# Kernel optimization log

Measured on AMD Instinct MI355X. Metric: run time of the kernel, lower is better.

The kernel has to match this reference:

```python
import jax, jax.numpy as jnp
from jax import lax
import numpy as np

B, S, H, L = 64, 512, 768, 9

def setup_inputs() -> dict:
    key = jax.random.key(0)
    ks = jax.random.split(key, 8)
    return {
        'hidden': jax.random.normal(ks[0], (B, S, H), dtype=jnp.float32),
        'W': jax.random.normal(ks[1], (H, L), dtype=jnp.float32) * 0.02,
        'b': jax.random.normal(ks[2], (L,), dtype=jnp.float32) * 0.02,
        'start_transitions': jax.random.normal(ks[3], (L,), dtype=jnp.float32) * 0.1,
        'transitions': jax.random.normal(ks[4], (L, L), dtype=jnp.float32) * 0.1,
        'end_transitions': jax.random.normal(ks[5], (L,), dtype=jnp.float32) * 0.1,
        'labels': jax.random.randint(ks[6], (B, S), 0, L, dtype=jnp.int64),
        'lengths': jax.random.randint(ks[7], (B,), 0, S, dtype=jnp.int32),
    }

def _crf_nll(emissions, labels, mask, start_transitions, transitions, end_transitions):
    # emissions [B,S,L], labels [B,S] int, mask [B,S] bool (mask[:,0] all True)
    Bv = emissions.shape[0]
    bidx = jnp.arange(Bv)
    fmask = mask.astype(emissions.dtype)
    # --- numerator: score of the gold path ---
    t0 = labels[:, 0]
    score0 = start_transitions[t0] + emissions[bidx, 0, t0]  # [B]
    def num_step(score, xs):
        em_t, tag_prev, tag_t, m_t = xs  # [B,L],[B],[B],[B]
        inc = transitions[tag_prev, tag_t] + em_t[bidx, tag_t]
        return score + inc * m_t, None
    num_xs = (jnp.swapaxes(emissions[:, 1:], 0, 1),  # [S-1,B,L]
              labels[:, :-1].T, labels[:, 1:].T, fmask[:, 1:].T)
    numerator, _ = lax.scan(num_step, score0, num_xs)
    seq_ends = jnp.sum(mask, axis=1) - 1  # [B]
    last_tags = labels[bidx, seq_ends]
    numerator = numerator + end_transitions[last_tags]
    # --- denominator: forward algorithm (logsumexp DP) ---
    alpha0 = start_transitions[None, :] + emissions[:, 0]  # [B,L]
    def den_step(alpha, xs):
        em_t, m_t = xs  # [B,L], [B] bool
        nxt = jax.scipy.special.logsumexp(
            alpha[:, :, None] + transitions[None, :, :] + em_t[:, None, :], axis=1)
        return jnp.where(m_t[:, None], nxt, alpha), None
    den_xs = (jnp.swapaxes(emissions[:, 1:], 0, 1), mask[:, 1:].T)
    alpha, _ = lax.scan(den_step, alpha0, den_xs)
    denominator = jax.scipy.special.logsumexp(alpha + end_transitions[None, :], axis=1)
    # torchcrf forward returns sum of log-likelihoods (reduction='sum'); model negates
    return -jnp.sum(numerator - denominator)

def reference(hidden, W, b, start_transitions, transitions, end_transitions, labels, lengths):
    # dropout is identity at inference; BERT output is modeled by `hidden`
    emissions = jnp.einsum('bsh,hl->bsl', hidden, W) + b  # [B,S,L]
    lens = jnp.maximum(lengths, 1)  # torchcrf requires mask[:,0] on
    mask = jnp.arange(emissions.shape[1])[None, :] < lens[:, None]  # [B,S]
    return _crf_nll(emissions, labels, mask, start_transitions, transitions, end_transitions)
```

## Files before the change

kernel.cpp:

```cpp
#include <hip/hip_runtime.h>

#define B_ 64
#define S_ 512
#define H_ 768
#define L_ 9
#define EMP 16
#define CH 16
#define NCHUNK 32
#define CPAD 88

typedef __attribute__((ext_vector_type(8))) short bf16x8;
typedef __attribute__((ext_vector_type(4))) float f32x4;

__device__ __forceinline__ int eoff(int t) { return t * 12 + (t >> 4) * 4; }

__device__ __forceinline__ unsigned pack_bf16(float lo, float hi) {
    unsigned a = __float_as_uint(lo) + 0x8000u;
    unsigned b = __float_as_uint(hi) + 0x8000u;
    return __builtin_amdgcn_perm(b, a, 0x07060302);
}

__global__ __launch_bounds__(256) void emis_kernel(
    const float* __restrict__ hidden, const float* __restrict__ W,
    const float* __restrict__ bias, const int* __restrict__ lengths,
    float* __restrict__ em, float* __restrict__ out)
{
    __shared__ unsigned Wl[96 * 16 * 4];
    __shared__ float bias16[16];

    const int T = threadIdx.x;
    if (blockIdx.x == 0 && T == 0) out[0] = 0.0f;

    const int row0 = blockIdx.x * 64;
    const int b = row0 >> 9;
    int len = lengths[b]; if (len < 1) len = 1;
    if ((row0 & 511) >= len) return;

    const int wv = T >> 6, lane = T & 63;
    const int r0 = row0 + wv * 16;
    const int q = lane >> 4, col = lane & 15;
    const bool tile_live = ((r0 & 511) < len);

    const float* hp = hidden + (size_t)(r0 + col) * H_ + q * 8;
    float4 ph[8];
    if (tile_live) {
        #pragma unroll
        for (int st = 0; st < 4; ++st) {
            ph[2 * st]     = *(const float4*)(hp + st * 32);
            ph[2 * st + 1] = *(const float4*)(hp + st * 32 + 4);
        }
    }

    if (T < 16) bias16[T] = (T < 9) ? bias[T] : 0.0f;
    #pragma unroll
    for (int r6 = 0; r6 < 6; ++r6) {
        const int sidx = T + 256 * r6;
        const int k8 = sidx >> 4, c = sidx & 15;
        unsigned w0 = 0, w1 = 0, w2 = 0, w3 = 0;
        if (c < 9) {
            const float* wp = W + (size_t)(k8 * 8) * 9 + c;
            w0 = pack_bf16(wp[0],  wp[9]);
            w1 = pack_bf16(wp[18], wp[27]);
            w2 = pack_bf16(wp[36], wp[45]);
            w3 = pack_bf16(wp[54], wp[63]);
        }
        uint4 v = { w0, w1, w2, w3 };
        *(uint4*)&Wl[sidx * 4] = v;
    }
    __syncthreads();

    if (!tile_live) return;

    const float4 bias4 = *(const float4*)(bias16 + q * 4);

    f32x4 acc = { 0.0f, 0.0f, 0.0f, 0.0f };
    #pragma unroll
    for (int st = 0; st < 24; ++st) {
        float4 h0, h1;
        if (st < 4) { h0 = ph[2 * st]; h1 = ph[2 * st + 1]; }
        else {
            h0 = *(const float4*)(hp + st * 32);
            h1 = *(const float4*)(hp + st * 32 + 4);
        }
        union { unsigned u[4]; bf16x8 v; } bu, au;
        bu.u[0] = pack_bf16(h0.x, h0.y);
        bu.u[1] = pack_bf16(h0.z, h0.w);
        bu.u[2] = pack_bf16(h1.x, h1.y);
        bu.u[3] = pack_bf16(h1.z, h1.w);
        const uint4 a4 = *(const uint4*)&Wl[((st * 4 + q) * 16 + col) * 4];
        au.u[0] = a4.x; au.u[1] = a4.y; au.u[2] = a4.z; au.u[3] = a4.w;
        acc = __builtin_amdgcn_mfma_f32_16x16x32_bf16(au.v, bu.v, acc, 0, 0, 0);
    }

    const int srow = (r0 & 511) + col;
    if (srow < len) {
        float4 o = { acc[0] + bias4.x, acc[1] + bias4.y,
                     acc[2] + bias4.z, acc[3] + bias4.w };
        *(float4*)(em + (size_t)((b << 9) + srow) * EMP + q * 4) = o;
    }
}

__global__ __launch_bounds__(384, 1) void crf_kernel(
    const float* __restrict__ em, const int* __restrict__ labels,
    const int* __restrict__ lengths, const float* __restrict__ start_t,
    const float* __restrict__ trans, const float* __restrict__ end_t,
    float* __restrict__ out)
{
    __shared__ float eem[6288];
    __shared__ float Pl[112];
    __shared__ float Cs[NCHUNK * CPAD];
    __shared__ float Cs2[16 * CPAD];
    __shared__ float rmx_s[16 * 12];
    __shared__ float lgA[32], lgB[16];
    const int T = threadIdx.x;
    const int b = blockIdx.x;
    int len = lengths[b]; if (len < 1) len = 1;

    if (T < 81) {
        const int k = T / 9, j = T - 9 * k;
        Pl[k * 12 + j] = __expf(trans[T]);
    }
    #pragma unroll
    for (int r = 0; r < 2; ++r) {
        const int t = T + 384 * r;
        if (t < len) {
            const int o = eoff(t);
            const float4* p = (const float4*)(em + (size_t)((b << 9) + t) * EMP);
            float4 v0 = p[0], v1 = p[1], v2 = p[2];
            float4 w0 = { __expf(v0.x), __expf(v0.y), __expf(v0.z), __expf(v0.w) };
            float4 w1 = { __expf(v1.x), __expf(v1.y), __expf(v1.z), __expf(v1.w) };
            *(float4*)(eem + o) = w0;
            *(float4*)(eem + o + 4) = w1;
            eem[o + 8] = __expf(v2.x);
        }
    }
    if (T < 32) lgA[T] = 0.0f;
    __syncthreads();

    if (T < 288) {
        const int c = T / 9;
        const int i = T - 9 * c;
        float A[9];
        #pragma unroll
        for (int j = 0; j < 9; ++j) A[j] = (i == j) ? 1.0f : 0.0f;
        const int t0 = CH * c + 1;

        #pragma unroll 1
        for (int s = 0; s < CH; ++s) {
            const int t = t0 + s;
            const int o = eoff(t);
            float4 e0 = *(const float4*)(eem + o);
            float4 e1 = *(const float4*)(eem + o + 4);
            const float e8 = eem[o + 8];
            const float e[9] = { e0.x, e0.y, e0.z, e0.w,
                                 e1.x, e1.y, e1.z, e1.w, e8 };

            float an[9];
            #pragma unroll
            for (int j = 0; j < 9; ++j) an[j] = 0.0f;
            #pragma unroll
            for (int k = 0; k < 9; ++k) {
                float4 p0 = *(const float4*)(Pl + k * 12);
                float4 p1 = *(const float4*)(Pl + k * 12 + 4);
                const float p8 = Pl[k * 12 + 8];
                const float pr[9] = { p0.x, p0.y, p0.z, p0.w,
                                      p1.x, p1.y, p1.z, p1.w, p8 };
                const float ak = A[k];
                #pragma unroll
                for (int j = 0; j < 9; ++j)
                    an[j] = fmaf(ak, pr[j], an[j]);
            }
            const bool live = (t < len);
            #pragma unroll
            for (int j = 0; j < 9; ++j)
                A[j] = live ? an[j] * e[j] : A[j];
            if (s == 7) {
                #pragma unroll
                for (int j = 0; j < 9; ++j) A[j] *= 0x1p-40f;
            }
        }
        #pragma unroll
        for (int j = 0; j < 9; ++j) Cs[c * CPAD + i * 9 + j] = A[j];
    } else if (T >= 320) {
        const int lane = T - 320;
        const int* lab = labels + (size_t)b * S_;
        float part = 0.0f;
        for (int t = 1 + lane; t < len; t += 64) {
            const int tp = lab[t - 1], tc = lab[t];
            part += trans[tp * 9 + tc] + em[(size_t)((b << 9) + t) * EMP + tc];
        }
        #pragma unroll
        for (int off = 32; off >= 1; off >>= 1) part += __shfl_xor(part, off, 64);
        if (lane == 0) {
            const int l0 = lab[0], le = lab[len - 1];
            const float num = start_t[l0] + em[(size_t)(b << 9) * EMP + l0]
                            + part + end_t[le];
            atomicAdd(out, -num);
        }
    }
    __syncthreads();

    float* src = Cs;  float* dst = Cs2;
    float* ls  = lgA; float* ld  = lgB;
    int nn = 16;
    #pragma unroll 1
    for (int lvl = 0; lvl < 5; ++lvl) {
        const int n = T / 9, i = T - 9 * n;
        float row[9];
        if (T < nn * 9) {
            const float* Am = src + (2 * n) * CPAD;
            const float* Bm = src + (2 * n + 1) * CPAD;
            float a[9];
            #pragma unroll
            for (int k = 0; k < 9; ++k) a[k] = Am[i * 9 + k];
            #pragma unroll
            for (int j = 0; j < 9; ++j) row[j] = 0.0f;
            #pragma unroll
            for (int k = 0; k < 9; ++k) {
                const float ak = a[k];
                #pragma unroll
                for (int j = 0; j < 9; ++j)
                    row[j] = fmaf(ak, Bm[k * 9 + j], row[j]);
            }
            float rmx = row[0];
            #pragma unroll
            for (int j = 1; j < 9; ++j) rmx = fmaxf(rmx, row[j]);
            rmx_s[n * 12 + i] = rmx;
        }
        __syncthreads();
        if (T < nn * 9) {
            float mx = rmx_s[n * 12];
            #pragma unroll
            for (int k = 1; k < 9; ++k) mx = fmaxf(mx, rmx_s[n * 12 + k]);
            const float inv = 1.0f / mx;
            #pragma unroll
            for (int j = 0; j < 9; ++j) dst[n * CPAD + i * 9 + j] = row[j] * inv;
            if (i == 0) ld[n] = ls[2 * n] + ls[2 * n + 1] + __logf(mx);
        }
        __syncthreads();
        float* t1 = src; src = dst; dst = t1;
        float* t2 = ls;  ls = ld;  ld = t2;
        nn >>= 1;
    }

    if (T == 0) {
        const float4* e0 = (const float4*)(em + (size_t)(b << 9) * EMP);
        float4 v0 = e0[0], v1 = e0[1], v2 = e0[2];
        float al[9] = { v0.x + start_t[0], v0.y + start_t[1], v0.z + start_t[2],
                        v0.w + start_t[3], v1.x + start_t[4], v1.y + start_t[5],
                        v1.z + start_t[6], v1.w + start_t[7], v2.x + start_t[8] };
        float m0 = al[0];
        #pragma unroll
        for (int j = 1; j < 9; ++j) m0 = fmaxf(m0, al[j]);
        float alpha[9];
        #pragma unroll
        for (int j = 0; j < 9; ++j) alpha[j] = __expf(al[j] - m0);

        float ev = 0.0f;
        #pragma unroll
        for (int j = 0; j < 9; ++j) {
            float s = 0.0f;
            #pragma unroll
            for (int i = 0; i < 9; ++i)
                s = fmaf(alpha[i], src[i * 9 + j], s);
            ev = fmaf(s, __expf(end_t[j]), ev);
        }
        const float den = m0 + ls[0] + __logf(ev)
                        + 1280.0f * 0.6931471805599453f;
        atomicAdd(out, den);
    }
}

extern "C" void kernel_launch(void* const* d_in, const int* in_sizes, int n_in,
                              void* d_out, int out_size, void* d_ws, size_t ws_size,
                              hipStream_t stream)
{
    (void)in_sizes; (void)n_in; (void)out_size; (void)ws_size;
    const float* hidden  = (const float*)d_in[0];
    const float* W       = (const float*)d_in[1];
    const float* bias    = (const float*)d_in[2];
    const float* start_t = (const float*)d_in[3];
    const float* trans   = (const float*)d_in[4];
    const float* end_t   = (const float*)d_in[5];
    const int*   labels  = (const int*)d_in[6];
    const int*   lengths = (const int*)d_in[7];

    float* em  = (float*)d_ws;
    float* out = (float*)d_out;

    emis_kernel<<<512, 256, 0, stream>>>(hidden, W, bias, lengths, em, out);
    crf_kernel<<<B_, 384, 0, stream>>>(em, labels, lengths,
                                       start_t, trans, end_t, out);
}
```

Measured before the change: 32.88 us.

## Split emission GEMM along hidden dim into two partial buffers summed in CRF

The emission kernel now splits the 768-wide reduction into two halves handled by separate blocks, doubling the grid to 1024 blocks. Each half writes a partial emission buffer, and the CRF kernel sums the two partials when it loads emissions. The aim is more parallelism and more memory requests in flight for the bandwidth-bound hidden read. The cost is extra workspace, twice the emission write and read traffic, and an extra add per element in the CRF kernel.

Measured after the change: 32.01 us, median of 2. 2.7% less time.

```diff
diff --git a/kernel.cpp b/kernel.cpp
--- a/kernel.cpp
+++ b/kernel.cpp
@@ -23,15 +23,17 @@
 __global__ __launch_bounds__(256) void emis_kernel(
     const float* __restrict__ hidden, const float* __restrict__ W,
     const float* __restrict__ bias, const int* __restrict__ lengths,
-    float* __restrict__ em, float* __restrict__ out)
+    float* __restrict__ em0, float* __restrict__ em1, float* __restrict__ out)
 {
-    __shared__ unsigned Wl[96 * 16 * 4];
+    __shared__ unsigned Wl[48 * 16 * 4];
     __shared__ float bias16[16];
 
     const int T = threadIdx.x;
     if (blockIdx.x == 0 && T == 0) out[0] = 0.0f;
 
-    const int row0 = blockIdx.x * 64;
+    const int kh  = blockIdx.x & 1;
+    const int grp = blockIdx.x >> 1;
+    const int row0 = grp * 64;
     const int b = row0 >> 9;
     int len = lengths[b]; if (len < 1) len = 1;
     if ((row0 & 511) >= len) return;
@@ -41,7 +43,7 @@
     const int q = lane >> 4, col = lane & 15;
     const bool tile_live = ((r0 & 511) < len);
 
-    const float* hp = hidden + (size_t)(r0 + col) * H_ + q * 8;
+    const float* hp = hidden + (size_t)(r0 + col) * H_ + kh * 384 + q * 8;
     float4 ph[8];
     if (tile_live) {
         #pragma unroll
@@ -51,14 +53,14 @@
         }
     }
 
-    if (T < 16) bias16[T] = (T < 9) ? bias[T] : 0.0f;
+    if (T < 16) bias16[T] = (kh == 0 && T < 9) ? bias[T] : 0.0f;
     #pragma unroll
-    for (int r6 = 0; r6 < 6; ++r6) {
-        const int sidx = T + 256 * r6;
-        const int k8 = sidx >> 4, c = sidx & 15;
+    for (int r3 = 0; r3 < 3; ++r3) {
+        const int sidx = T + 256 * r3;
+        const int k8l = sidx >> 4, c = sidx & 15;
         unsigned w0 = 0, w1 = 0, w2 = 0, w3 = 0;
         if (c < 9) {
-            const float* wp = W + (size_t)(k8 * 8) * 9 + c;
+            const float* wp = W + (size_t)(kh * 384 + k8l * 8) * 9 + c;
             w0 = pack_bf16(wp[0],  wp[9]);
             w1 = pack_bf16(wp[18], wp[27]);
             w2 = pack_bf16(wp[36], wp[45]);
@@ -75,7 +77,7 @@
 
     f32x4 acc = { 0.0f, 0.0f, 0.0f, 0.0f };
     #pragma unroll
-    for (int st = 0; st < 24; ++st) {
+    for (int st = 0; st < 12; ++st) {
         float4 h0, h1;
         if (st < 4) { h0 = ph[2 * st]; h1 = ph[2 * st + 1]; }
         else {
@@ -94,17 +96,18 @@
 
     const int srow = (r0 & 511) + col;
     if (srow < len) {
+        float* dst = (kh ? em1 : em0) + (size_t)((b << 9) + srow) * EMP + q * 4;
         float4 o = { acc[0] + bias4.x, acc[1] + bias4.y,
                      acc[2] + bias4.z, acc[3] + bias4.w };
-        *(float4*)(em + (size_t)((b << 9) + srow) * EMP + q * 4) = o;
+        *(float4*)dst = o;
     }
 }
 
 __global__ __launch_bounds__(384, 1) void crf_kernel(
-    const float* __restrict__ em, const int* __restrict__ labels,
-    const int* __restrict__ lengths, const float* __restrict__ start_t,
-    const float* __restrict__ trans, const float* __restrict__ end_t,
-    float* __restrict__ out)
+    const float* __restrict__ em0, const float* __restrict__ em1,
+    const int* __restrict__ labels, const int* __restrict__ lengths,
+    const float* __restrict__ start_t, const float* __restrict__ trans,
+    const float* __restrict__ end_t, float* __restrict__ out)
 {
     __shared__ float eem[6288];
     __shared__ float Pl[112];
@@ -125,13 +128,18 @@
         const int t = T + 384 * r;
         if (t < len) {
             const int o = eoff(t);
-            const float4* p = (const float4*)(em + (size_t)((b << 9) + t) * EMP);
-            float4 v0 = p[0], v1 = p[1], v2 = p[2];
-            float4 w0 = { __expf(v0.x), __expf(v0.y), __expf(v0.z), __expf(v0.w) };
-            float4 w1 = { __expf(v1.x), __expf(v1.y), __expf(v1.z), __expf(v1.w) };
+            const size_t off = (size_t)((b << 9) + t) * EMP;
+            const float4* p0 = (const float4*)(em0 + off);
+            const float4* p1 = (const float4*)(em1 + off);
+            float4 a0 = p0[0], a1 = p0[1], a2 = p0[2];
+            float4 b0 = p1[0], b1 = p1[1], b2 = p1[2];
+            float4 w0 = { __expf(a0.x + b0.x), __expf(a0.y + b0.y),
+                          __expf(a0.z + b0.z), __expf(a0.w + b0.w) };
+            float4 w1 = { __expf(a1.x + b1.x), __expf(a1.y + b1.y),
+                          __expf(a1.z + b1.z), __expf(a1.w + b1.w) };
             *(float4*)(eem + o) = w0;
             *(float4*)(eem + o + 4) = w1;
-            eem[o + 8] = __expf(v2.x);
+            eem[o + 8] = __expf(a2.x + b2.x);
         }
     }
     if (T < 32) lgA[T] = 0.0f;
@@ -187,13 +195,15 @@
         float part = 0.0f;
         for (int t = 1 + lane; t < len; t += 64) {
             const int tp = lab[t - 1], tc = lab[t];
-            part += trans[tp * 9 + tc] + em[(size_t)((b << 9) + t) * EMP + tc];
+            const size_t idx = (size_t)((b << 9) + t) * EMP + tc;
+            part += trans[tp * 9 + tc] + em0[idx] + em1[idx];
         }
         #pragma unroll
         for (int off = 32; off >= 1; off >>= 1) part += __shfl_xor(part, off, 64);
         if (lane == 0) {
             const int l0 = lab[0], le = lab[len - 1];
-            const float num = start_t[l0] + em[(size_t)(b << 9) * EMP + l0]
+            const size_t i0 = (size_t)(b << 9) * EMP + l0;
+            const float num = start_t[l0] + em0[i0] + em1[i0]
                             + part + end_t[le];
             atomicAdd(out, -num);
         }
@@ -244,11 +254,16 @@
     }
 
     if (T == 0) {
-        const float4* e0 = (const float4*)(em + (size_t)(b << 9) * EMP);
-        float4 v0 = e0[0], v1 = e0[1], v2 = e0[2];
-        float al[9] = { v0.x + start_t[0], v0.y + start_t[1], v0.z + start_t[2],
-                        v0.w + start_t[3], v1.x + start_t[4], v1.y + start_t[5],
-                        v1.z + start_t[6], v1.w + start_t[7], v2.x + start_t[8] };
+        const size_t off0 = (size_t)(b << 9) * EMP;
+        const float4* p0 = (const float4*)(em0 + off0);
+        const float4* p1 = (const float4*)(em1 + off0);
+        float4 a0 = p0[0], a1 = p0[1], a2 = p0[2];
+        float4 b0 = p1[0], b1 = p1[1], b2 = p1[2];
+        float al[9] = { a0.x + b0.x + start_t[0], a0.y + b0.y + start_t[1],
+                        a0.z + b0.z + start_t[2], a0.w + b0.w + start_t[3],
+                        a1.x + b1.x + start_t[4], a1.y + b1.y + start_t[5],
+                        a1.z + b1.z + start_t[6], a1.w + b1.w + start_t[7],
+                        a2.x + b2.x + start_t[8] };
         float m0 = al[0];
         #pragma unroll
         for (int j = 1; j < 9; ++j) m0 = fmaxf(m0, al[j]);
@@ -285,10 +300,12 @@
     const int*   labels  = (const int*)d_in[6];
     const int*   lengths = (const int*)d_in[7];
 
-    float* em  = (float*)d_ws;
+    float* em0 = (float*)d_ws;
+    float* em1 = em0 + (size_t)B_ * S_ * EMP;
     float* out = (float*)d_out;
 
-    emis_kernel<<<512, 256, 0, stream>>>(hidden, W, bias, lengths, em, out);
-    crf_kernel<<<B_, 384, 0, stream>>>(em, labels, lengths,
+    emis_kernel<<<1024, 256, 0, stream>>>(hidden, W, bias, lengths,
+                                          em0, em1, out);
+    crf_kernel<<<B_, 384, 0, stream>>>(em0, em1, labels, lengths,
                                        start_t, trans, end_t, out);
 }
```

## Fuse CRF chunk transfer-matrix products and gold-path scoring into emission kernel

Applied to the files above, without the earlier changes.

The per-chunk 9x9 transfer-matrix products and the numerator (gold-path) partial sums now run inside the emission GEMM blocks, straight from emissions held in shared memory. Each block writes 4 chunk matrices and a numerator partial to workspace. The CRF kernel then only loads the chunk matrices, substituting scaled identity matrices for dead chunks, and runs the log-depth tree reduction. This removes the round trip of the full emission tensor through global memory and the serial per-chunk loop in the 64-block CRF kernel, at the cost of longer emission blocks and an extra small workspace read.

New measurement: 32.60 us (median of 2 runs). About the same (-0.8%).

```diff
diff --git a/kernel.cpp b/kernel.cpp
--- a/kernel.cpp
+++ b/kernel.cpp
@@ -4,15 +4,10 @@
 #define S_ 512
 #define H_ 768
 #define L_ 9
-#define EMP 16
-#define CH 16
-#define NCHUNK 32
 #define CPAD 88
 
 typedef __attribute__((ext_vector_type(8))) short bf16x8;
 typedef __attribute__((ext_vector_type(4))) float f32x4;
-
-__device__ __forceinline__ int eoff(int t) { return t * 12 + (t >> 4) * 4; }
 
 __device__ __forceinline__ unsigned pack_bf16(float lo, float hi) {
     unsigned a = __float_as_uint(lo) + 0x8000u;
@@ -23,22 +18,31 @@
 __global__ __launch_bounds__(256) void emis_kernel(
     const float* __restrict__ hidden, const float* __restrict__ W,
     const float* __restrict__ bias, const int* __restrict__ lengths,
-    float* __restrict__ em, float* __restrict__ out)
+    const int* __restrict__ labels, const float* __restrict__ start_t,
+    const float* __restrict__ trans, const float* __restrict__ end_t,
+    float* __restrict__ Crec, float* __restrict__ em_row0,
+    float* __restrict__ num_part, float* __restrict__ out)
 {
     __shared__ unsigned Wl[96 * 16 * 4];
+    __shared__ float em_t[64 * 12];
+    __shared__ float ee_t[64 * 12];
+    __shared__ float Pl[112];
     __shared__ float bias16[16];
 
     const int T = threadIdx.x;
-    if (blockIdx.x == 0 && T == 0) out[0] = 0.0f;
-
-    const int row0 = blockIdx.x * 64;
-    const int b = row0 >> 9;
+    const int g = blockIdx.x;
+    const int b = g >> 3;
+    const int s0 = (g & 7) * 64;
+    if (g == 0 && T == 0) out[0] = 0.0f;
     int len = lengths[b]; if (len < 1) len = 1;
-    if ((row0 & 511) >= len) return;
+    if (s0 >= len) {
+        if (T == 0) num_part[g] = 0.0f;
+        return;
+    }
 
     const int wv = T >> 6, lane = T & 63;
-    const int r0 = row0 + wv * 16;
     const int q = lane >> 4, col = lane & 15;
+    const int r0 = g * 64 + wv * 16;
     const bool tile_live = ((r0 & 511) < len);
 
     const float* hp = hidden + (size_t)(r0 + col) * H_ + q * 8;
@@ -52,6 +56,7 @@
     }
 
     if (T < 16) bias16[T] = (T < 9) ? bias[T] : 0.0f;
+    if (T < 81) Pl[(T / 9) * 12 + (T % 9)] = __expf(trans[T]);
     #pragma unroll
     for (int r6 = 0; r6 < 6; ++r6) {
         const int sidx = T + 256 * r6;
@@ -69,92 +74,60 @@
     }
     __syncthreads();
 
-    if (!tile_live) return;
-
-    const float4 bias4 = *(const float4*)(bias16 + q * 4);
-
-    f32x4 acc = { 0.0f, 0.0f, 0.0f, 0.0f };
-    #pragma unroll
-    for (int st = 0; st < 24; ++st) {
-        float4 h0, h1;
-        if (st < 4) { h0 = ph[2 * st]; h1 = ph[2 * st + 1]; }
-        else {
-            h0 = *(const float4*)(hp + st * 32);
-            h1 = *(const float4*)(hp + st * 32 + 4);
-        }
-        union { unsigned u[4]; bf16x8 v; } bu, au;
-        bu.u[0] = pack_bf16(h0.x, h0.y);
-        bu.u[1] = pack_bf16(h0.z, h0.w);
-        bu.u[2] = pack_bf16(h1.x, h1.y);
-        bu.u[3] = pack_bf16(h1.z, h1.w);
-        const uint4 a4 = *(const uint4*)&Wl[((st * 4 + q) * 16 + col) * 4];
-        au.u[0] = a4.x; au.u[1] = a4.y; au.u[2] = a4.z; au.u[3] = a4.w;
-        acc = __builtin_amdgcn_mfma_f32_16x16x32_bf16(au.v, bu.v, acc, 0, 0, 0);
-    }
-
-    const int srow = (r0 & 511) + col;
-    if (srow < len) {
-        float4 o = { acc[0] + bias4.x, acc[1] + bias4.y,
-                     acc[2] + bias4.z, acc[3] + bias4.w };
-        *(float4*)(em + (size_t)((b << 9) + srow) * EMP + q * 4) = o;
-    }
-}
-
-__global__ __launch_bounds__(384, 1) void crf_kernel(
-    const float* __restrict__ em, const int* __restrict__ labels,
-    const int* __restrict__ lengths, const float* __restrict__ start_t,
-    const float* __restrict__ trans, const float* __restrict__ end_t,
-    float* __restrict__ out)
-{
-    __shared__ float eem[6288];
-    __shared__ float Pl[112];
-    __shared__ float Cs[NCHUNK * CPAD];
-    __shared__ float Cs2[16 * CPAD];
-    __shared__ float rmx_s[16 * 12];
-    __shared__ float lgA[32], lgB[16];
-    const int T = threadIdx.x;
-    const int b = blockIdx.x;
-    int len = lengths[b]; if (len < 1) len = 1;
-
-    if (T < 81) {
-        const int k = T / 9, j = T - 9 * k;
-        Pl[k * 12 + j] = __expf(trans[T]);
-    }
-    #pragma unroll
-    for (int r = 0; r < 2; ++r) {
-        const int t = T + 384 * r;
-        if (t < len) {
-            const int o = eoff(t);
-            const float4* p = (const float4*)(em + (size_t)((b << 9) + t) * EMP);
-            float4 v0 = p[0], v1 = p[1], v2 = p[2];
-            float4 w0 = { __expf(v0.x), __expf(v0.y), __expf(v0.z), __expf(v0.w) };
-            float4 w1 = { __expf(v1.x), __expf(v1.y), __expf(v1.z), __expf(v1.w) };
-            *(float4*)(eem + o) = w0;
-            *(float4*)(eem + o + 4) = w1;
-            eem[o + 8] = __expf(v2.x);
-        }
-    }
-    if (T < 32) lgA[T] = 0.0f;
+    if (tile_live) {
+        f32x4 acc = { 0.0f, 0.0f, 0.0f, 0.0f };
+        #pragma unroll
+        for (int st = 0; st < 24; ++st) {
+            float4 h0, h1;
+            if (st < 4) { h0 = ph[2 * st]; h1 = ph[2 * st + 1]; }
+            else {
+                h0 = *(const float4*)(hp + st * 32);
+                h1 = *(const float4*)(hp + st * 32 + 4);
+            }
+            union { unsigned u[4]; bf16x8 v; } bu, au;
+            bu.u[0] = pack_bf16(h0.x, h0.y);
+            bu.u[1] = pack_bf16(h0.z, h0.w);
+            bu.u[2] = pack_bf16(h1.x, h1.y);
+            bu.u[3] = pack_bf16(h1.z, h1.w);
+            const uint4 a4 = *(const uint4*)&Wl[((st * 4 + q) * 16 + col) * 4];
+            au.u[0] = a4.x; au.u[1] = a4.y; au.u[2] = a4.z; au.u[3] = a4.w;
+            acc = __builtin_amdgcn_mfma_f32_16x16x32_bf16(au.v, bu.v, acc, 0, 0, 0);
+        }
+        if (q < 3) {
+            const float4 b4 = *(const float4*)(bias16 + q * 4);
+            float4 o = { acc[0] + b4.x, acc[1] + b4.y,
+                         acc[2] + b4.z, acc[3] + b4.w };
+            *(float4*)&em_t[(wv * 16 + col) * 12 + q * 4] = o;
+        }
+    }
     __syncthreads();
 
-    if (T < 288) {
-        const int c = T / 9;
-        const int i = T - 9 * c;
+    if (T < 192) {
+        #pragma unroll
+        for (int k = 0; k < 3; ++k) {
+            const int idx = T + 192 * k;
+            const int r = idx / 9, c = idx - 9 * r;
+            ee_t[r * 12 + c] = __expf(em_t[r * 12 + c]);
+        }
+    }
+    __syncthreads();
+
+    if (T < 36) {
+        const int cl = T / 9, i = T - 9 * cl;
+        const int cg = 4 * (g & 7) + cl;
         float A[9];
         #pragma unroll
         for (int j = 0; j < 9; ++j) A[j] = (i == j) ? 1.0f : 0.0f;
-        const int t0 = CH * c + 1;
 
         #pragma unroll 1
-        for (int s = 0; s < CH; ++s) {
-            const int t = t0 + s;
-            const int o = eoff(t);
-            float4 e0 = *(const float4*)(eem + o);
-            float4 e1 = *(const float4*)(eem + o + 4);
-            const float e8 = eem[o + 8];
+        for (int s = 0; s < 16; ++s) {
+            const int t = 16 * cg + s;
+            const int r = 16 * cl + s;
+            float4 e0 = *(const float4*)&ee_t[r * 12];
+            float4 e1 = *(const float4*)&ee_t[r * 12 + 4];
+            const float e8 = ee_t[r * 12 + 8];
             const float e[9] = { e0.x, e0.y, e0.z, e0.w,
                                  e1.x, e1.y, e1.z, e1.w, e8 };
-
             float an[9];
             #pragma unroll
             for (int j = 0; j < 9; ++j) an[j] = 0.0f;
@@ -170,7 +143,7 @@
                 for (int j = 0; j < 9; ++j)
                     an[j] = fmaf(ak, pr[j], an[j]);
             }
-            const bool live = (t < len);
+            const bool live = (t >= 1) && (t < len);
             #pragma unroll
             for (int j = 0; j < 9; ++j)
                 A[j] = live ? an[j] * e[j] : A[j];
@@ -179,25 +152,60 @@
                 for (int j = 0; j < 9; ++j) A[j] *= 0x1p-40f;
             }
         }
-        #pragma unroll
-        for (int j = 0; j < 9; ++j) Cs[c * CPAD + i * 9 + j] = A[j];
-    } else if (T >= 320) {
-        const int lane = T - 320;
-        const int* lab = labels + (size_t)b * S_;
+        float* rec = Crec + ((size_t)b * 32 + cg) * CPAD + i * 9;
+        #pragma unroll
+        for (int j = 0; j < 9; ++j) rec[j] = A[j];
+    } else if (T >= 36 && T < 45) {
+        if (s0 == 0) em_row0[b * 12 + (T - 36)] = em_t[T - 36];
+    } else if (T >= 64 && T < 128) {
+        const int ln = T - 64;
+        const int t = s0 + ln;
         float part = 0.0f;
-        for (int t = 1 + lane; t < len; t += 64) {
-            const int tp = lab[t - 1], tc = lab[t];
-            part += trans[tp * 9 + tc] + em[(size_t)((b << 9) + t) * EMP + tc];
+        if (t >= 1 && t < len) {
+            const int tp = labels[b * S_ + t - 1];
+            const int tc = labels[b * S_ + t];
+            part = trans[tp * 9 + tc] + em_t[ln * 12 + tc];
+        }
+        if (ln == 0) {
+            if (s0 == 0) {
+                const int l0 = labels[b * S_];
+                part += start_t[l0] + em_t[l0];
+            }
+            if (s0 <= len - 1 && len - 1 < s0 + 64)
+                part += end_t[labels[b * S_ + len - 1]];
         }
         #pragma unroll
         for (int off = 32; off >= 1; off >>= 1) part += __shfl_xor(part, off, 64);
-        if (lane == 0) {
-            const int l0 = lab[0], le = lab[len - 1];
-            const float num = start_t[l0] + em[(size_t)(b << 9) * EMP + l0]
-                            + part + end_t[le];
-            atomicAdd(out, -num);
-        }
-    }
+        if (ln == 0) num_part[g] = part;
+    }
+}
+
+__global__ __launch_bounds__(192, 1) void crf_kernel(
+    const float* __restrict__ Crec, const float* __restrict__ em_row0,
+    const float* __restrict__ num_part, const int* __restrict__ lengths,
+    const float* __restrict__ start_t, const float* __restrict__ end_t,
+    float* __restrict__ out)
+{
+    __shared__ float Cs[32 * CPAD];
+    __shared__ float Cs2[16 * CPAD];
+    __shared__ float rmx_s[16 * 12];
+    __shared__ float lgA[32], lgB[16];
+    const int T = threadIdx.x;
+    const int b = blockIdx.x;
+    int len = lengths[b]; if (len < 1) len = 1;
+
+    if (T < 96) {
+        const int c = T / 3, p = T - 3 * (T / 3);
+        const bool ownerLive = ((c >> 2) * 64) < len;
+        const float* rec = Crec + ((size_t)b * 32 + c) * CPAD + p * 27;
+        #pragma unroll
+        for (int k = 0; k < 27; ++k) {
+            const int i = 3 * p + k / 9, j = k % 9;
+            Cs[c * CPAD + p * 27 + k] =
+                ownerLive ? rec[k] : ((i == j) ? 0x1p-40f : 0.0f);
+        }
+    }
+    if (T < 32) lgA[T] = 0.0f;
     __syncthreads();
 
     float* src = Cs;  float* dst = Cs2;
@@ -244,11 +252,9 @@
     }
 
     if (T == 0) {
-        const float4* e0 = (const float4*)(em + (size_t)(b << 9) * EMP);
-        float4 v0 = e0[0], v1 = e0[1], v2 = e0[2];
-        float al[9] = { v0.x + start_t[0], v0.y + start_t[1], v0.z + start_t[2],
-                        v0.w + start_t[3], v1.x + start_t[4], v1.y + start_t[5],
-                        v1.z + start_t[6], v1.w + start_t[7], v2.x + start_t[8] };
+        float al[9];
+        #pragma unroll
+        for (int j = 0; j < 9; ++j) al[j] = em_row0[b * 12 + j] + start_t[j];
         float m0 = al[0];
         #pragma unroll
         for (int j = 1; j < 9; ++j) m0 = fmaxf(m0, al[j]);
@@ -267,7 +273,10 @@
         }
         const float den = m0 + ls[0] + __logf(ev)
                         + 1280.0f * 0.6931471805599453f;
-        atomicAdd(out, den);
+        float num = 0.0f;
+        #pragma unroll
+        for (int k = 0; k < 8; ++k) num += num_part[b * 8 + k];
+        atomicAdd(out, den - num);
     }
 }
 
@@ -285,10 +294,14 @@
     const int*   labels  = (const int*)d_in[6];
     const int*   lengths = (const int*)d_in[7];
 
-    float* em  = (float*)d_ws;
-    float* out = (float*)d_out;
-
-    emis_kernel<<<512, 256, 0, stream>>>(hidden, W, bias, lengths, em, out);
-    crf_kernel<<<B_, 384, 0, stream>>>(em, labels, lengths,
-                                       start_t, trans, end_t, out);
+    float* Crec     = (float*)d_ws;
+    float* em_row0  = Crec + (size_t)64 * 32 * CPAD;
+    float* num_part = em_row0 + 64 * 12;
+    float* out      = (float*)d_out;
+
+    emis_kernel<<<512, 256, 0, stream>>>(hidden, W, bias, lengths, labels,
+                                         start_t, trans, end_t,
+                                         Crec, em_row0, num_part, out);
+    crf_kernel<<<B_, 192, 0, stream>>>(Crec, em_row0, num_part, lengths,
+                                       start_t, end_t, out);
 }
```

## Coalesce hidden loads via LDS staging with double-buffered register prefetch

Applied to the files above, without the earlier changes.

Changes the emission GEMM kernel so each wave loads hidden rows with lanes spanning contiguous 64-float segments (coalesced), converts them to bf16, and stages them in a per-wave double-buffered LDS tile that the MFMA then reads in fragment layout. Loads for two steps ahead are held in registers to overlap global latency with the MFMAs. The aim is to cut the strided per-lane global access pattern of the previous layout, at the cost of extra LDS traffic and shared memory. It relies on wave-local LDS ordering with no explicit barrier.

Result: faster. 31.47 us (-4.3%).

```diff
diff --git a/kernel.cpp b/kernel.cpp
--- a/kernel.cpp
+++ b/kernel.cpp
@@ -11,6 +11,8 @@
 
 typedef __attribute__((ext_vector_type(8))) short bf16x8;
 typedef __attribute__((ext_vector_type(4))) float f32x4;
+typedef bf16x8 __attribute__((may_alias)) bf16x8_a;
+typedef uint2  __attribute__((may_alias)) uint2_a;
 
 __device__ __forceinline__ int eoff(int t) { return t * 12 + (t >> 4) * 4; }
 
@@ -27,28 +29,30 @@
 {
     __shared__ unsigned Wl[96 * 16 * 4];
     __shared__ float bias16[16];
+    __shared__ unsigned hbuf[4][2][16 * 36];
 
     const int T = threadIdx.x;
     if (blockIdx.x == 0 && T == 0) out[0] = 0.0f;
 
-    const int row0 = blockIdx.x * 64;
-    const int b = row0 >> 9;
+    const int g = blockIdx.x;
+    const int b = g >> 3;
     int len = lengths[b]; if (len < 1) len = 1;
-    if ((row0 & 511) >= len) return;
+    if (((g & 7) * 64) >= len) return;
 
     const int wv = T >> 6, lane = T & 63;
-    const int r0 = row0 + wv * 16;
     const int q = lane >> 4, col = lane & 15;
+    const int r0 = g * 64 + wv * 16;
     const bool tile_live = ((r0 & 511) < len);
 
-    const float* hp = hidden + (size_t)(r0 + col) * H_ + q * 8;
-    float4 ph[8];
+    const int srow = lane >> 2, sm = lane & 3;
+    const float* hrow = hidden + (size_t)(r0 + srow) * H_ + sm * 4;
+
+    float4 L[2][4];
     if (tile_live) {
         #pragma unroll
-        for (int st = 0; st < 4; ++st) {
-            ph[2 * st]     = *(const float4*)(hp + st * 32);
-            ph[2 * st + 1] = *(const float4*)(hp + st * 32 + 4);
-        }
+        for (int m = 0; m < 4; ++m) L[0][m] = *(const float4*)(hrow + m * 16);
+        #pragma unroll
+        for (int m = 0; m < 4; ++m) L[1][m] = *(const float4*)(hrow + 64 + m * 16);
     }
 
     if (T < 16) bias16[T] = (T < 9) ? bias[T] : 0.0f;
@@ -71,32 +75,57 @@
 
     if (!tile_live) return;
 
+    unsigned* buf0 = &hbuf[wv][0][0];
+    unsigned* buf1 = &hbuf[wv][1][0];
+    const int woff = srow * 36 + sm * 2;
+    const int rdoff = col * 36 + q * 4;
+
+    #pragma unroll
+    for (int m = 0; m < 4; ++m) {
+        uint2 u = { pack_bf16(L[0][m].x, L[0][m].y),
+                    pack_bf16(L[0][m].z, L[0][m].w) };
+        *(uint2_a*)(buf0 + woff + m * 8) = u;
+    }
+
     const float4 bias4 = *(const float4*)(bias16 + q * 4);
-
     f32x4 acc = { 0.0f, 0.0f, 0.0f, 0.0f };
+
     #pragma unroll
-    for (int st = 0; st < 24; ++st) {
-        float4 h0, h1;
-        if (st < 4) { h0 = ph[2 * st]; h1 = ph[2 * st + 1]; }
-        else {
-            h0 = *(const float4*)(hp + st * 32);
-            h1 = *(const float4*)(hp + st * 32 + 4);
-        }
-        union { unsigned u[4]; bf16x8 v; } bu, au;
-        bu.u[0] = pack_bf16(h0.x, h0.y);
-        bu.u[1] = pack_bf16(h0.z, h0.w);
-        bu.u[2] = pack_bf16(h1.x, h1.y);
-        bu.u[3] = pack_bf16(h1.z, h1.w);
-        const uint4 a4 = *(const uint4*)&Wl[((st * 4 + q) * 16 + col) * 4];
-        au.u[0] = a4.x; au.u[1] = a4.y; au.u[2] = a4.z; au.u[3] = a4.w;
-        acc = __builtin_amdgcn_mfma_f32_16x16x32_bf16(au.v, bu.v, acc, 0, 0, 0);
-    }
-
-    const int srow = (r0 & 511) + col;
-    if (srow < len) {
+    for (int p = 0; p < 12; ++p) {
+        unsigned* cbuf = (p & 1) ? buf1 : buf0;
+        unsigned* nbuf = (p & 1) ? buf0 : buf1;
+
+        if (p + 2 < 12) {
+            #pragma unroll
+            for (int m = 0; m < 4; ++m)
+                L[p & 1][m] = *(const float4*)(hrow + (p + 2) * 64 + m * 16);
+        }
+
+        #pragma unroll
+        for (int s = 0; s < 2; ++s) {
+            const bf16x8 bu = *(const bf16x8_a*)(cbuf + rdoff + s * 16);
+            const uint4 a4 =
+                *(const uint4*)&Wl[(((p * 2 + s) * 4 + q) * 16 + col) * 4];
+            union { unsigned u[4]; bf16x8 v; } au;
+            au.u[0] = a4.x; au.u[1] = a4.y; au.u[2] = a4.z; au.u[3] = a4.w;
+            acc = __builtin_amdgcn_mfma_f32_16x16x32_bf16(au.v, bu, acc, 0, 0, 0);
+        }
+
+        if (p + 1 < 12) {
+            #pragma unroll
+            for (int m = 0; m < 4; ++m) {
+                uint2 u = { pack_bf16(L[(p + 1) & 1][m].x, L[(p + 1) & 1][m].y),
+                            pack_bf16(L[(p + 1) & 1][m].z, L[(p + 1) & 1][m].w) };
+                *(uint2_a*)(nbuf + woff + m * 8) = u;
+            }
+        }
+    }
+
+    const int srow_out = (r0 & 511) + col;
+    if (srow_out < len) {
         float4 o = { acc[0] + bias4.x, acc[1] + bias4.y,
                      acc[2] + bias4.z, acc[3] + bias4.w };
-        *(float4*)(em + (size_t)((b << 9) + srow) * EMP + q * 4) = o;
+        *(float4*)(em + (size_t)((b << 9) + srow_out) * EMP + q * 4) = o;
     }
 }
 
```
